# Performance work log

Measured on AMD Instinct MI355X. Metric: run time of the kernel, lower is better.

Reference implementation:

```python
import jax, jax.numpy as jnp
import numpy as np

HEADS = 4
DIM_HEAD = 32
GROUPS = 32  # min(256//4, 32)
EPS = 1e-5


def setup_inputs() -> dict:
    key = jax.random.key(0)
    ks = jax.random.split(key, 5)
    B, C, H, W = 16, 256, 64, 64
    CD, HC, WC = 512, 32, 32
    hid = HEADS * DIM_HEAD  # 128
    return {
        "x": jax.random.normal(ks[0], (B, C, H, W), jnp.float32),
        "cond": jax.random.normal(ks[1], (B, CD, HC, WC), jnp.float32),
        "gn_w": jnp.ones((C,), jnp.float32),
        "gn_b": jnp.zeros((C,), jnp.float32),
        "w_q": jax.random.normal(ks[2], (hid, C), jnp.float32) * 0.05,
        "b_q": jnp.zeros((hid,), jnp.float32),
        "w_kv": jax.random.normal(ks[3], (2 * hid, CD), jnp.float32) * 0.05,
        "b_kv": jnp.zeros((2 * hid,), jnp.float32),
        "w_out": jax.random.normal(ks[4], (C, hid), jnp.float32) * 0.05,
        "b_out": jnp.zeros((C,), jnp.float32),
    }


def _group_norm(x, w, b):
    # x: (B, C, H, W); normalize per group over (channels-in-group, H, W)
    B, C, H, W = x.shape
    xg = x.reshape(B, GROUPS, C // GROUPS, H, W)
    mu = jnp.mean(xg, axis=(2, 3, 4), keepdims=True)
    var = jnp.var(xg, axis=(2, 3, 4), keepdims=True)
    xn = ((xg - mu) * jax.lax.rsqrt(var + EPS)).reshape(B, C, H, W)
    return xn * w[None, :, None, None] + b[None, :, None, None]


def _conv1x1(x, w, b):
    # x: (B, Cin, H, W), w: (Cout, Cin), b: (Cout,)
    return jnp.einsum('oc,bchw->bohw', w, x) + b[None, :, None, None]


def reference(x, cond, gn_w, gn_b, w_q, b_q, w_kv, b_kv, w_out, b_out):
    B, C, H, W = x.shape
    hid = HEADS * DIM_HEAD
    xn = _group_norm(x, gn_w, gn_b)
    q = _conv1x1(xn, w_q, b_q)          # (B, hid, H, W)
    kv = _conv1x1(cond, w_kv, b_kv)     # (B, 2*hid, Hc, Wc)
    Nc = kv.shape[2] * kv.shape[3]
    N = H * W
    k = kv[:, :hid].reshape(B, HEADS, DIM_HEAD, Nc)
    v = kv[:, hid:].reshape(B, HEADS, DIM_HEAD, Nc)
    q = q.reshape(B, HEADS, DIM_HEAD, N)
    k = jax.nn.softmax(k, axis=-1)
    # kv outer product: (B, heads, d, e)
    context = jnp.einsum('bhdn,bhen->bhde', k, v)
    # query contraction over d: (B, heads, e, n)
    out = jnp.einsum('bhde,bhdn->bhen', context, q)
    out = out.reshape(B, hid, H, W)
    return _conv1x1(out, w_out, b_out)
```

## Files before the change

kernel.cpp:

```cpp
#include <hip/hip_runtime.h>
#include <hip/hip_bf16.h>

typedef __attribute__((ext_vector_type(8))) short bf16x8;
typedef __attribute__((ext_vector_type(4))) float f32x4;

__device__ __forceinline__ ushort f2bf(float f) {
    __hip_bfloat16 h = __float2bfloat16(f);
    return __builtin_bit_cast(ushort, h);
}
__device__ __forceinline__ float bflo(unsigned u) { return __uint_as_float(u << 16); }
__device__ __forceinline__ float bfhi(unsigned u) { return __uint_as_float(u & 0xffff0000u); }

__device__ __forceinline__ void unpack8(uint4 r, float* o) {
    o[0] = bflo(r.x); o[1] = bfhi(r.x); o[2] = bflo(r.y); o[3] = bfhi(r.y);
    o[4] = bflo(r.z); o[5] = bfhi(r.z); o[6] = bflo(r.w); o[7] = bfhi(r.w);
}

__device__ __forceinline__ void gload16(const void* g, void* l) {
    __builtin_amdgcn_global_load_lds(
        (const __attribute__((address_space(1))) unsigned*)g,
        (__attribute__((address_space(3))) unsigned*)l,
        16, 0, 0);
}

__global__ void cvtw_kernel(const float* __restrict__ w, ushort* __restrict__ o,
                            float* __restrict__ zbase) {
    int i = blockIdx.x * 256 + threadIdx.x;
    if (i < 68608) zbase[i] = 0.f;
    o[i] = f2bf(w[i]);
}

template<int C, int NPIX, bool STATS>
__device__ __forceinline__ void tconv_body(const float* __restrict__ in,
                                           ushort* __restrict__ outp,
                                           float* __restrict__ statacc,
                                           int b, int c0, int n0) {
    __shared__ ushort tile[64][68];
    __shared__ float gacc[8][2];
    const float* ip = in + (size_t)b * C * NPIX;
    ushort* op = outp + (size_t)b * NPIX * C;
    int t = threadIdx.x;
    if (STATS) {
        if (t < 16) gacc[t >> 1][t & 1] = 0.f;
        __syncthreads();
    }
    float sj[4], ssj[4];
    #pragma unroll
    for (int j = 0; j < 4; ++j) {
        int e = t + 256 * j;
        int cc = e >> 4, q = e & 15;
        float4 v = *(const float4*)&ip[(size_t)(c0 + cc) * NPIX + n0 + q * 4];
        ushort4 u;
        u.x = f2bf(v.x); u.y = f2bf(v.y); u.z = f2bf(v.z); u.w = f2bf(v.w);
        *(ushort4*)&tile[cc][q * 4] = u;
        if (STATS) {
            sj[j]  = v.x + v.y + v.z + v.w;
            ssj[j] = v.x*v.x + v.y*v.y + v.z*v.z + v.w*v.w;
        }
    }
    if (STATS) {
        #pragma unroll
        for (int j = 0; j < 4; ++j) {
            #pragma unroll
            for (int off = 1; off < 16; off <<= 1) {
                sj[j]  += __shfl_xor(sj[j], off, 64);
                ssj[j] += __shfl_xor(ssj[j], off, 64);
            }
        }
        if ((t & 15) == 0) {
            #pragma unroll
            for (int j = 0; j < 4; ++j) {
                int cc = (t >> 4) + 16 * j;
                atomicAdd(&gacc[cc >> 3][0], sj[j]);
                atomicAdd(&gacc[cc >> 3][1], ssj[j]);
            }
        }
    }
    __syncthreads();
    #pragma unroll
    for (int j = 0; j < 4; ++j) {
        int e = t + 256 * j;
        int nn = e >> 4, q = e & 15;
        ushort4 u;
        u.x = tile[q*4+0][nn]; u.y = tile[q*4+1][nn];
        u.z = tile[q*4+2][nn]; u.w = tile[q*4+3][nn];
        *(ushort4*)&op[(size_t)(n0 + nn) * C + c0 + q * 4] = u;
    }
    if (STATS && t < 8) {
        int g = b * 32 + (c0 >> 3) + t;
        atomicAdd(&statacc[g * 2],     gacc[t][0]);
        atomicAdd(&statacc[g * 2 + 1], gacc[t][1]);
    }
}

__global__ __launch_bounds__(256) void tpose_kernel(const float* __restrict__ x,
                                                    const float* __restrict__ cond,
                                                    ushort* __restrict__ xT,
                                                    ushort* __restrict__ condT,
                                                    float* __restrict__ statacc) {
    int bid = blockIdx.x;
    if (bid < 4096) {
        int b = bid >> 8, rem = bid & 255;
        tconv_body<256, 4096, true>(x, xT, statacc, b, (rem >> 6) * 64, (rem & 63) * 64);
    } else {
        int id = bid - 4096;
        int b = id >> 7, rem = id & 127;
        tconv_body<512, 1024, false>(cond, condT, nullptr, b, (rem >> 4) * 64, (rem & 15) * 64);
    }
}

template<int K, int N, bool OUTF32>
__global__ __launch_bounds__(256) void nt_gemm(const ushort* __restrict__ Amat, long long strideA,
                                               const ushort* __restrict__ Bmat, long long strideB,
                                               const float* __restrict__ biasv, int strideBias,
                                               void* __restrict__ Cmat, long long strideC) {
    __shared__ ushort lA[128 * 64];
    __shared__ ushort lB[128 * 64];
    int b = blockIdx.z;
    int col0 = blockIdx.x * 128, row0 = blockIdx.y * 128;
    int t = threadIdx.x;
    int l = t & 63, wid = t >> 6;
    int wr = wid >> 1, wc = wid & 1;
    int lr = l & 15, lg = l >> 4;
    const ushort* Ab = Amat + (size_t)b * strideA + (size_t)row0 * K;
    const ushort* Bb = Bmat + (size_t)b * strideB + (size_t)col0 * K;
    f32x4 acc[4][4] = {};
    for (int k0 = 0; k0 < K; k0 += 64) {
        #pragma unroll
        for (int j = 0; j < 4; ++j) {
            int gi = j * 256 + t;
            int r = gi >> 3, g = (gi & 7) ^ (r & 7);
            gload16(Ab + (size_t)r * K + k0 + g * 8, (char*)lA + gi * 16);
        }
        #pragma unroll
        for (int j = 0; j < 4; ++j) {
            int gi = j * 256 + t;
            int r = gi >> 3, g = (gi & 7) ^ (r & 7);
            gload16(Bb + (size_t)r * K + k0 + g * 8, (char*)lB + gi * 16);
        }
        __syncthreads();
        #pragma unroll
        for (int ks = 0; ks < 2; ++ks) {
            bf16x8 av[4], bv[4];
            #pragma unroll
            for (int mi = 0; mi < 4; ++mi) {
                int ar = wr * 64 + mi * 16 + lr;
                int q = (ks * 4 + lg) ^ (ar & 7);
                av[mi] = *(const bf16x8*)((const char*)lA + ar * 128 + q * 16);
            }
            #pragma unroll
            for (int ni = 0; ni < 4; ++ni) {
                int br = wc * 64 + ni * 16 + lr;
                int q = (ks * 4 + lg) ^ (br & 7);
                bv[ni] = *(const bf16x8*)((const char*)lB + br * 128 + q * 16);
            }
            #pragma unroll
            for (int mi = 0; mi < 4; ++mi)
                #pragma unroll
                for (int ni = 0; ni < 4; ++ni)
                    acc[mi][ni] = __builtin_amdgcn_mfma_f32_16x16x32_bf16(
                        av[mi], bv[ni], acc[mi][ni], 0, 0, 0);
        }
        __syncthreads();
    }
    const float* bp = biasv + (size_t)b * strideBias;
    int orow = row0 + wr * 64, ocol = col0 + wc * 64 + lr;
    #pragma unroll
    for (int mi = 0; mi < 4; ++mi) {
        int rb = orow + mi * 16 + lg * 4;
        float4 b4 = *(const float4*)&bp[rb];
        float bvr[4] = {b4.x, b4.y, b4.z, b4.w};
        #pragma unroll
        for (int ni = 0; ni < 4; ++ni) {
            int cc = ocol + ni * 16;
            #pragma unroll
            for (int r = 0; r < 4; ++r) {
                float v = acc[mi][ni][r] + bvr[r];
                if constexpr (OUTF32)
                    ((float*)Cmat + (size_t)b * strideC)[(size_t)(rb + r) * N + cc] = v;
                else
                    ((ushort*)Cmat + (size_t)b * strideC)[(size_t)(rb + r) * N + cc] = f2bf(v);
            }
        }
    }
}

template<int K, int N, bool OUTF32>
__global__ __launch_bounds__(256) void nt_gemm64(const ushort* __restrict__ Amat, long long strideA,
                                                 const ushort* __restrict__ Bmat, long long strideB,
                                                 const float* __restrict__ biasv, int strideBias,
                                                 void* __restrict__ Cmat, long long strideC) {
    __shared__ ushort lA[64 * 64];
    __shared__ ushort lB[64 * 64];
    int b = blockIdx.z;
    int col0 = blockIdx.x * 64, row0 = blockIdx.y * 64;
    int t = threadIdx.x;
    int l = t & 63, wid = t >> 6;
    int wr = wid >> 1, wc = wid & 1;
    int lr = l & 15, lg = l >> 4;
    const ushort* Ab = Amat + (size_t)b * strideA + (size_t)row0 * K;
    const ushort* Bb = Bmat + (size_t)b * strideB + (size_t)col0 * K;
    f32x4 acc[2][2] = {};
    for (int k0 = 0; k0 < K; k0 += 64) {
        #pragma unroll
        for (int j = 0; j < 2; ++j) {
            int gi = j * 256 + t;
            int r = gi >> 3, g = (gi & 7) ^ (r & 7);
            gload16(Ab + (size_t)r * K + k0 + g * 8, (char*)lA + gi * 16);
        }
        #pragma unroll
        for (int j = 0; j < 2; ++j) {
            int gi = j * 256 + t;
            int r = gi >> 3, g = (gi & 7) ^ (r & 7);
            gload16(Bb + (size_t)r * K + k0 + g * 8, (char*)lB + gi * 16);
        }
        __syncthreads();
        #pragma unroll
        for (int ks = 0; ks < 2; ++ks) {
            bf16x8 av[2], bv[2];
            #pragma unroll
            for (int mi = 0; mi < 2; ++mi) {
                int ar = wr * 32 + mi * 16 + lr;
                int q = (ks * 4 + lg) ^ (ar & 7);
                av[mi] = *(const bf16x8*)((const char*)lA + ar * 128 + q * 16);
            }
            #pragma unroll
            for (int ni = 0; ni < 2; ++ni) {
                int br = wc * 32 + ni * 16 + lr;
                int q = (ks * 4 + lg) ^ (br & 7);
                bv[ni] = *(const bf16x8*)((const char*)lB + br * 128 + q * 16);
            }
            #pragma unroll
            for (int mi = 0; mi < 2; ++mi)
                #pragma unroll
                for (int ni = 0; ni < 2; ++ni)
                    acc[mi][ni] = __builtin_amdgcn_mfma_f32_16x16x32_bf16(
                        av[mi], bv[ni], acc[mi][ni], 0, 0, 0);
        }
        __syncthreads();
    }
    const float* bp = biasv + (size_t)b * strideBias;
    int orow = row0 + wr * 32, ocol = col0 + wc * 32 + lr;
    #pragma unroll
    for (int mi = 0; mi < 2; ++mi) {
        int rb = orow + mi * 16 + lg * 4;
        float4 b4 = *(const float4*)&bp[rb];
        float bvr[4] = {b4.x, b4.y, b4.z, b4.w};
        #pragma unroll
        for (int ni = 0; ni < 2; ++ni) {
            int cc = ocol + ni * 16;
            #pragma unroll
            for (int r = 0; r < 4; ++r) {
                float v = acc[mi][ni][r] + bvr[r];
                if constexpr (OUTF32)
                    ((float*)Cmat + (size_t)b * strideC)[(size_t)(rb + r) * N + cc] = v;
                else
                    ((ushort*)Cmat + (size_t)b * strideC)[(size_t)(rb + r) * N + cc] = f2bf(v);
            }
        }
    }
}

__global__ __launch_bounds__(256) void ctx_partial_kernel(const ushort* __restrict__ kv,
                                                          float* __restrict__ rowsum,
                                                          float* __restrict__ ctx) {
    int bh = blockIdx.y, b = bh >> 2, h = bh & 3;
    int n0 = blockIdx.x * 128;
    __shared__ float pl[32][129], vl[32][129];
    int t = threadIdx.x;
    int r = t >> 3, cs = (t & 7) * 16;
    const ushort* kp = kv + ((size_t)b * 256 + h * 32 + r) * 1024 + n0 + cs;
    const ushort* vp = kv + ((size_t)b * 256 + 128 + h * 32 + r) * 1024 + n0 + cs;
    float kvals[16], vvals[16];
    unpack8(((const uint4*)kp)[0], kvals);
    unpack8(((const uint4*)kp)[1], kvals + 8);
    unpack8(((const uint4*)vp)[0], vvals);
    unpack8(((const uint4*)vp)[1], vvals + 8);
    float psum = 0.f;
    #pragma unroll
    for (int i = 0; i < 16; ++i) {
        float e = __expf(kvals[i]);
        pl[r][cs + i] = e;
        vl[r][cs + i] = vvals[i];
        psum += e;
    }
    psum += __shfl_xor(psum, 1, 64);
    psum += __shfl_xor(psum, 2, 64);
    psum += __shfl_xor(psum, 4, 64);
    if ((t & 7) == 0) atomicAdd(&rowsum[bh * 32 + r], psum);
    __syncthreads();
    int d0 = t >> 5, e0 = t & 31;
    float acc[4] = {0.f, 0.f, 0.f, 0.f};
    #pragma unroll 8
    for (int nn = 0; nn < 128; ++nn) {
        float vv = vl[e0][nn];
        #pragma unroll
        for (int i = 0; i < 4; ++i)
            acc[i] += pl[d0 + 8 * i][nn] * vv;
    }
    #pragma unroll
    for (int i = 0; i < 4; ++i)
        atomicAdd(&ctx[((size_t)bh * 32 + d0 + 8 * i) * 32 + e0], acc[i]);
}

__global__ __launch_bounds__(256) void a_kernel(const float* __restrict__ ctx,
                                                const float* __restrict__ rowsum,
                                                const float* __restrict__ w_out,
                                                const float* __restrict__ w_q,
                                                const float* __restrict__ b_q,
                                                const float* __restrict__ statacc,
                                                const float* __restrict__ gn_w,
                                                const float* __restrict__ gn_b,
                                                const float* __restrict__ b_out,
                                                ushort* __restrict__ A16,
                                                float* __restrict__ biasb) {
    __shared__ float ctxl[4][32][33];
    __shared__ float wol[16][128];
    __shared__ float ml[16][128];
    __shared__ float cbuf[256][17];
    __shared__ float pbuf[16][17];
    int b = blockIdx.x >> 4, ot = (blockIdx.x & 15) << 4;
    int t = threadIdx.x;
    #pragma unroll
    for (int j = 0; j < 16; ++j) {
        int e = t + 256 * j;
        float inv = 1.f / rowsum[b * 128 + (e >> 5)];
        ctxl[e >> 10][(e >> 5) & 31][e & 31] = ctx[(size_t)b * 4096 + e] * inv;
    }
    #pragma unroll
    for (int j = 0; j < 8; ++j) {
        int e = t + 256 * j;
        wol[e >> 7][e & 127] = w_out[(ot + (e >> 7)) * 128 + (e & 127)];
    }
    __syncthreads();
    #pragma unroll
    for (int j = 0; j < 8; ++j) {
        int e = t + 256 * j;
        int o = e >> 7, hd = e & 127, h = hd >> 5, d = hd & 31;
        float acc = 0.f;
        #pragma unroll
        for (int ee = 0; ee < 32; ++ee) acc += wol[o][h * 32 + ee] * ctxl[h][d][ee];
        ml[o][hd] = acc;
    }
    __syncthreads();
    int c = t, g = c >> 3;
    float a0 = statacc[(b * 32 + g) * 2], a1 = statacc[(b * 32 + g) * 2 + 1];
    float mu  = a0 * (1.f / 32768.f);
    float var = a1 * (1.f / 32768.f) - mu * mu;
    float sc = rsqrtf(var + 1e-5f) * gn_w[c];
    float tc = gn_b[c] - mu * sc;
    float wt[16];
    #pragma unroll
    for (int o = 0; o < 16; ++o) wt[o] = 0.f;
    for (int hd = 0; hd < 128; ++hd) {
        float wq = w_q[hd * 256 + c];
        #pragma unroll
        for (int o = 0; o < 16; ++o) wt[o] += ml[o][hd] * wq;
    }
    ushort* Abp = A16 + ((size_t)b * 256 + ot) * 256 + c;
    #pragma unroll
    for (int o = 0; o < 16; ++o) {
        Abp[(size_t)o * 256] = f2bf(wt[o] * sc);
        cbuf[c][o] = wt[o] * tc;
    }
    __syncthreads();
    {
        int o = t >> 4, seg = t & 15;
        float p = 0.f;
        #pragma unroll
        for (int i = 0; i < 16; ++i) p += cbuf[seg * 16 + i][o];
        pbuf[o][seg] = p;
    }
    __syncthreads();
    if (t < 16) {
        int o = t;
        float sum = 0.f;
        #pragma unroll
        for (int s2 = 0; s2 < 16; ++s2) sum += pbuf[o][s2];
        float md = 0.f;
        #pragma unroll 8
        for (int hd = 0; hd < 128; ++hd) md += ml[o][hd] * b_q[hd];
        biasb[(size_t)b * 256 + ot + o] = sum + md + b_out[ot + o];
    }
}

extern "C" void kernel_launch(void* const* d_in, const int* in_sizes, int n_in,
                              void* d_out, int out_size, void* d_ws, size_t ws_size,
                              hipStream_t stream) {
    const float* x     = (const float*)d_in[0];
    const float* cond  = (const float*)d_in[1];
    const float* gn_w  = (const float*)d_in[2];
    const float* gn_b  = (const float*)d_in[3];
    const float* w_q   = (const float*)d_in[4];
    const float* b_q   = (const float*)d_in[5];
    const float* w_kv  = (const float*)d_in[6];
    const float* b_kv  = (const float*)d_in[7];
    const float* w_out = (const float*)d_in[8];
    const float* b_out = (const float*)d_in[9];
    float* out = (float*)d_out;

    float* f       = (float*)d_ws;
    float* statacc = f;
    float* rowsum  = f + 1024;
    float* ctx     = f + 3072;
    float* biasb   = f + 68608;
    ushort* u      = (ushort*)(f + 72704);
    ushort* wkv16  = u;
    ushort* kv16   = u + 131072;
    ushort* A16    = u + 4325376;
    ushort* xT     = u + 5373952;
    ushort* condT  = u + 22151168;

    cvtw_kernel<<<512, 256, 0, stream>>>(w_kv, wkv16, statacc);
    tpose_kernel<<<6144, 256, 0, stream>>>(x, cond, xT, condT, statacc);
    nt_gemm64<512, 1024, false><<<dim3(16, 4, 16), 256, 0, stream>>>(
        wkv16, 0, condT, (long long)512 * 1024, b_kv, 0, kv16, (long long)256 * 1024);
    ctx_partial_kernel<<<dim3(8, 64), 256, 0, stream>>>(kv16, rowsum, ctx);
    a_kernel<<<256, 256, 0, stream>>>(ctx, rowsum, w_out, w_q, b_q, statacc,
                                      gn_w, gn_b, b_out, A16, biasb);
    nt_gemm<256, 4096, true><<<dim3(32, 2, 16), 256, 0, stream>>>(
        A16, 65536, xT, (long long)4096 * 256, biasb, 256, out, (long long)256 * 4096);
}
```

Before: 90.60 us.

## Fuse fp32-to-bf16 transpose into GEMM loaders and drop transpose kernel

Removes the separate transpose/convert kernel that wrote bf16 transposed copies of x and cond. Both GEMMs now read fp32 activations directly, convert them to bf16 and transpose into swizzled LDS inside the K loop. The kv GEMM kernel also computes group-norm statistics in extra blocks that read x once per group. This removes a large round-trip write and read of transposed intermediates. In exchange the loads are synchronous register loads rather than async LDS loads, and the output GEMM now uses a 256x128 tile with 512 threads.

Result: no change. 91.13 us (+0.6%).

```diff
diff --git a/kernel.cpp b/kernel.cpp
--- a/kernel.cpp
+++ b/kernel.cpp
@@ -30,233 +30,106 @@
     o[i] = f2bf(w[i]);
 }
 
-template<int C, int NPIX, bool STATS>
-__device__ __forceinline__ void tconv_body(const float* __restrict__ in,
-                                           ushort* __restrict__ outp,
-                                           float* __restrict__ statacc,
-                                           int b, int c0, int n0) {
-    __shared__ ushort tile[64][68];
-    __shared__ float gacc[8][2];
-    const float* ip = in + (size_t)b * C * NPIX;
-    ushort* op = outp + (size_t)b * NPIX * C;
-    int t = threadIdx.x;
-    if (STATS) {
-        if (t < 16) gacc[t >> 1][t & 1] = 0.f;
-        __syncthreads();
-    }
-    float sj[4], ssj[4];
-    #pragma unroll
-    for (int j = 0; j < 4; ++j) {
-        int e = t + 256 * j;
-        int cc = e >> 4, q = e & 15;
-        float4 v = *(const float4*)&ip[(size_t)(c0 + cc) * NPIX + n0 + q * 4];
-        ushort4 u;
-        u.x = f2bf(v.x); u.y = f2bf(v.y); u.z = f2bf(v.z); u.w = f2bf(v.w);
-        *(ushort4*)&tile[cc][q * 4] = u;
-        if (STATS) {
-            sj[j]  = v.x + v.y + v.z + v.w;
-            ssj[j] = v.x*v.x + v.y*v.y + v.z*v.z + v.w*v.w;
-        }
-    }
-    if (STATS) {
-        #pragma unroll
-        for (int j = 0; j < 4; ++j) {
-            #pragma unroll
-            for (int off = 1; off < 16; off <<= 1) {
-                sj[j]  += __shfl_xor(sj[j], off, 64);
-                ssj[j] += __shfl_xor(ssj[j], off, 64);
-            }
-        }
-        if ((t & 15) == 0) {
-            #pragma unroll
-            for (int j = 0; j < 4; ++j) {
-                int cc = (t >> 4) + 16 * j;
-                atomicAdd(&gacc[cc >> 3][0], sj[j]);
-                atomicAdd(&gacc[cc >> 3][1], ssj[j]);
-            }
-        }
-    }
-    __syncthreads();
-    #pragma unroll
-    for (int j = 0; j < 4; ++j) {
-        int e = t + 256 * j;
-        int nn = e >> 4, q = e & 15;
-        ushort4 u;
-        u.x = tile[q*4+0][nn]; u.y = tile[q*4+1][nn];
-        u.z = tile[q*4+2][nn]; u.w = tile[q*4+3][nn];
-        *(ushort4*)&op[(size_t)(n0 + nn) * C + c0 + q * 4] = u;
-    }
-    if (STATS && t < 8) {
-        int g = b * 32 + (c0 >> 3) + t;
-        atomicAdd(&statacc[g * 2],     gacc[t][0]);
-        atomicAdd(&statacc[g * 2 + 1], gacc[t][1]);
-    }
-}
-
-__global__ __launch_bounds__(256) void tpose_kernel(const float* __restrict__ x,
-                                                    const float* __restrict__ cond,
-                                                    ushort* __restrict__ xT,
-                                                    ushort* __restrict__ condT,
-                                                    float* __restrict__ statacc) {
-    int bid = blockIdx.x;
-    if (bid < 4096) {
-        int b = bid >> 8, rem = bid & 255;
-        tconv_body<256, 4096, true>(x, xT, statacc, b, (rem >> 6) * 64, (rem & 63) * 64);
-    } else {
-        int id = bid - 4096;
-        int b = id >> 7, rem = id & 127;
-        tconv_body<512, 1024, false>(cond, condT, nullptr, b, (rem >> 4) * 64, (rem & 15) * 64);
-    }
-}
-
-template<int K, int N, bool OUTF32>
-__global__ __launch_bounds__(256) void nt_gemm(const ushort* __restrict__ Amat, long long strideA,
-                                               const ushort* __restrict__ Bmat, long long strideB,
-                                               const float* __restrict__ biasv, int strideBias,
-                                               void* __restrict__ Cmat, long long strideC) {
-    __shared__ ushort lA[128 * 64];
-    __shared__ ushort lB[128 * 64];
-    int b = blockIdx.z;
-    int col0 = blockIdx.x * 128, row0 = blockIdx.y * 128;
-    int t = threadIdx.x;
-    int l = t & 63, wid = t >> 6;
-    int wr = wid >> 1, wc = wid & 1;
-    int lr = l & 15, lg = l >> 4;
-    const ushort* Ab = Amat + (size_t)b * strideA + (size_t)row0 * K;
-    const ushort* Bb = Bmat + (size_t)b * strideB + (size_t)col0 * K;
-    f32x4 acc[4][4] = {};
-    for (int k0 = 0; k0 < K; k0 += 64) {
-        #pragma unroll
-        for (int j = 0; j < 4; ++j) {
-            int gi = j * 256 + t;
-            int r = gi >> 3, g = (gi & 7) ^ (r & 7);
-            gload16(Ab + (size_t)r * K + k0 + g * 8, (char*)lA + gi * 16);
-        }
-        #pragma unroll
-        for (int j = 0; j < 4; ++j) {
-            int gi = j * 256 + t;
-            int r = gi >> 3, g = (gi & 7) ^ (r & 7);
-            gload16(Bb + (size_t)r * K + k0 + g * 8, (char*)lB + gi * 16);
-        }
-        __syncthreads();
-        #pragma unroll
-        for (int ks = 0; ks < 2; ++ks) {
-            bf16x8 av[4], bv[4];
-            #pragma unroll
-            for (int mi = 0; mi < 4; ++mi) {
-                int ar = wr * 64 + mi * 16 + lr;
-                int q = (ks * 4 + lg) ^ (ar & 7);
-                av[mi] = *(const bf16x8*)((const char*)lA + ar * 128 + q * 16);
-            }
-            #pragma unroll
-            for (int ni = 0; ni < 4; ++ni) {
-                int br = wc * 64 + ni * 16 + lr;
-                int q = (ks * 4 + lg) ^ (br & 7);
-                bv[ni] = *(const bf16x8*)((const char*)lB + br * 128 + q * 16);
-            }
-            #pragma unroll
-            for (int mi = 0; mi < 4; ++mi)
-                #pragma unroll
-                for (int ni = 0; ni < 4; ++ni)
-                    acc[mi][ni] = __builtin_amdgcn_mfma_f32_16x16x32_bf16(
-                        av[mi], bv[ni], acc[mi][ni], 0, 0, 0);
-        }
-        __syncthreads();
-    }
-    const float* bp = biasv + (size_t)b * strideBias;
-    int orow = row0 + wr * 64, ocol = col0 + wc * 64 + lr;
-    #pragma unroll
-    for (int mi = 0; mi < 4; ++mi) {
-        int rb = orow + mi * 16 + lg * 4;
-        float4 b4 = *(const float4*)&bp[rb];
-        float bvr[4] = {b4.x, b4.y, b4.z, b4.w};
-        #pragma unroll
-        for (int ni = 0; ni < 4; ++ni) {
-            int cc = ocol + ni * 16;
-            #pragma unroll
-            for (int r = 0; r < 4; ++r) {
-                float v = acc[mi][ni][r] + bvr[r];
-                if constexpr (OUTF32)
-                    ((float*)Cmat + (size_t)b * strideC)[(size_t)(rb + r) * N + cc] = v;
-                else
-                    ((ushort*)Cmat + (size_t)b * strideC)[(size_t)(rb + r) * N + cc] = f2bf(v);
-            }
-        }
-    }
-}
-
-template<int K, int N, bool OUTF32>
-__global__ __launch_bounds__(256) void nt_gemm64(const ushort* __restrict__ Amat, long long strideA,
-                                                 const ushort* __restrict__ Bmat, long long strideB,
-                                                 const float* __restrict__ biasv, int strideBias,
-                                                 void* __restrict__ Cmat, long long strideC) {
+__global__ __launch_bounds__(256) void kvstats_kernel(const ushort* __restrict__ wkv16,
+                                                      const float* __restrict__ cond,
+                                                      const float* __restrict__ b_kv,
+                                                      ushort* __restrict__ kv16,
+                                                      const float* __restrict__ x,
+                                                      float* __restrict__ statacc) {
     __shared__ ushort lA[64 * 64];
     __shared__ ushort lB[64 * 64];
-    int b = blockIdx.z;
-    int col0 = blockIdx.x * 64, row0 = blockIdx.y * 64;
+    __shared__ float ls[4], lss[4];
+    int bid = blockIdx.x;
     int t = threadIdx.x;
-    int l = t & 63, wid = t >> 6;
-    int wr = wid >> 1, wc = wid & 1;
-    int lr = l & 15, lg = l >> 4;
-    const ushort* Ab = Amat + (size_t)b * strideA + (size_t)row0 * K;
-    const ushort* Bb = Bmat + (size_t)b * strideB + (size_t)col0 * K;
-    f32x4 acc[2][2] = {};
-    for (int k0 = 0; k0 < K; k0 += 64) {
-        #pragma unroll
-        for (int j = 0; j < 2; ++j) {
-            int gi = j * 256 + t;
-            int r = gi >> 3, g = (gi & 7) ^ (r & 7);
-            gload16(Ab + (size_t)r * K + k0 + g * 8, (char*)lA + gi * 16);
-        }
-        #pragma unroll
-        for (int j = 0; j < 2; ++j) {
-            int gi = j * 256 + t;
-            int r = gi >> 3, g = (gi & 7) ^ (r & 7);
-            gload16(Bb + (size_t)r * K + k0 + g * 8, (char*)lB + gi * 16);
-        }
+    if (bid < 1024) {
+        int nb = bid & 15, ob = (bid >> 4) & 3, b = bid >> 6;
+        int col0 = nb * 64, row0 = ob * 64;
+        int l = t & 63, wid = t >> 6;
+        int wr = wid >> 1, wc = wid & 1;
+        int lr = l & 15, lg = l >> 4;
+        const ushort* Ab = wkv16 + (size_t)row0 * 512;
+        const float* Bb = cond + (size_t)b * 512 * 1024;
+        int sp = t & 31, sj = t >> 5;
+        f32x4 acc[2][2] = {};
+        for (int k0 = 0; k0 < 512; k0 += 64) {
+            #pragma unroll
+            for (int j = 0; j < 2; ++j) {
+                int gi = j * 256 + t;
+                int r = gi >> 3, g = (gi & 7) ^ (r & 7);
+                gload16(Ab + (size_t)r * 512 + k0 + g * 8, (char*)lA + gi * 16);
+            }
+            const float* r0 = Bb + (size_t)(k0 + 2 * sp) * 1024 + col0 + sj * 8;
+            float4 v0a = *(const float4*)r0;
+            float4 v0b = *(const float4*)(r0 + 4);
+            float4 v1a = *(const float4*)(r0 + 1024);
+            float4 v1b = *(const float4*)(r0 + 1028);
+            float c0v[8] = {v0a.x, v0a.y, v0a.z, v0a.w, v0b.x, v0b.y, v0b.z, v0b.w};
+            float c1v[8] = {v1a.x, v1a.y, v1a.z, v1a.w, v1b.x, v1b.y, v1b.z, v1b.w};
+            #pragma unroll
+            for (int w = 0; w < 8; ++w) {
+                int n = sj * 8 + w;
+                unsigned pk = (unsigned)f2bf(c0v[w]) | ((unsigned)f2bf(c1v[w]) << 16);
+                *(unsigned*)((char*)lB + n * 128 + (((sp >> 2) ^ (n & 7)) * 16) + (sp & 3) * 4) = pk;
+            }
+            __syncthreads();
+            #pragma unroll
+            for (int ks = 0; ks < 2; ++ks) {
+                bf16x8 av[2], bv[2];
+                #pragma unroll
+                for (int mi = 0; mi < 2; ++mi) {
+                    int ar = wr * 32 + mi * 16 + lr;
+                    int q = (ks * 4 + lg) ^ (ar & 7);
+                    av[mi] = *(const bf16x8*)((const char*)lA + ar * 128 + q * 16);
+                }
+                #pragma unroll
+                for (int ni = 0; ni < 2; ++ni) {
+                    int br = wc * 32 + ni * 16 + lr;
+                    int q = (ks * 4 + lg) ^ (br & 7);
+                    bv[ni] = *(const bf16x8*)((const char*)lB + br * 128 + q * 16);
+                }
+                #pragma unroll
+                for (int mi = 0; mi < 2; ++mi)
+                    #pragma unroll
+                    for (int ni = 0; ni < 2; ++ni)
+                        acc[mi][ni] = __builtin_amdgcn_mfma_f32_16x16x32_bf16(
+                            av[mi], bv[ni], acc[mi][ni], 0, 0, 0);
+            }
+            __syncthreads();
+        }
+        int orow = row0 + wr * 32, ocol = col0 + wc * 32 + lr;
+        #pragma unroll
+        for (int mi = 0; mi < 2; ++mi) {
+            int rb = orow + mi * 16 + lg * 4;
+            float4 b4 = *(const float4*)&b_kv[rb];
+            float bvr[4] = {b4.x, b4.y, b4.z, b4.w};
+            #pragma unroll
+            for (int ni = 0; ni < 2; ++ni) {
+                int cc = ocol + ni * 16;
+                #pragma unroll
+                for (int r = 0; r < 4; ++r)
+                    kv16[((size_t)b * 256 + rb + r) * 1024 + cc] = f2bf(acc[mi][ni][r] + bvr[r]);
+            }
+        }
+    } else {
+        int bg = bid - 1024;
+        const float4* xp = (const float4*)(x + (size_t)bg * 32768);
+        float s = 0.f, ss = 0.f;
+        for (int i = t; i < 8192; i += 256) {
+            float4 v = xp[i];
+            s  += v.x + v.y + v.z + v.w;
+            ss += v.x*v.x + v.y*v.y + v.z*v.z + v.w*v.w;
+        }
+        #pragma unroll
+        for (int off = 32; off > 0; off >>= 1) {
+            s  += __shfl_down(s, off, 64);
+            ss += __shfl_down(ss, off, 64);
+        }
+        int wave = t >> 6;
+        if ((t & 63) == 0) { ls[wave] = s; lss[wave] = ss; }
         __syncthreads();
-        #pragma unroll
-        for (int ks = 0; ks < 2; ++ks) {
-            bf16x8 av[2], bv[2];
-            #pragma unroll
-            for (int mi = 0; mi < 2; ++mi) {
-                int ar = wr * 32 + mi * 16 + lr;
-                int q = (ks * 4 + lg) ^ (ar & 7);
-                av[mi] = *(const bf16x8*)((const char*)lA + ar * 128 + q * 16);
-            }
-            #pragma unroll
-            for (int ni = 0; ni < 2; ++ni) {
-                int br = wc * 32 + ni * 16 + lr;
-                int q = (ks * 4 + lg) ^ (br & 7);
-                bv[ni] = *(const bf16x8*)((const char*)lB + br * 128 + q * 16);
-            }
-            #pragma unroll
-            for (int mi = 0; mi < 2; ++mi)
-                #pragma unroll
-                for (int ni = 0; ni < 2; ++ni)
-                    acc[mi][ni] = __builtin_amdgcn_mfma_f32_16x16x32_bf16(
-                        av[mi], bv[ni], acc[mi][ni], 0, 0, 0);
-        }
-        __syncthreads();
-    }
-    const float* bp = biasv + (size_t)b * strideBias;
-    int orow = row0 + wr * 32, ocol = col0 + wc * 32 + lr;
-    #pragma unroll
-    for (int mi = 0; mi < 2; ++mi) {
-        int rb = orow + mi * 16 + lg * 4;
-        float4 b4 = *(const float4*)&bp[rb];
-        float bvr[4] = {b4.x, b4.y, b4.z, b4.w};
-        #pragma unroll
-        for (int ni = 0; ni < 2; ++ni) {
-            int cc = ocol + ni * 16;
-            #pragma unroll
-            for (int r = 0; r < 4; ++r) {
-                float v = acc[mi][ni][r] + bvr[r];
-                if constexpr (OUTF32)
-                    ((float*)Cmat + (size_t)b * strideC)[(size_t)(rb + r) * N + cc] = v;
-                else
-                    ((ushort*)Cmat + (size_t)b * strideC)[(size_t)(rb + r) * N + cc] = f2bf(v);
-            }
+        if (t == 0) {
+            statacc[bg * 2]     = ls[0] + ls[1] + ls[2] + ls[3];
+            statacc[bg * 2 + 1] = lss[0] + lss[1] + lss[2] + lss[3];
         }
     }
 }
@@ -384,6 +257,84 @@
     }
 }
 
+__global__ __launch_bounds__(512) void out_gemm_fused(const ushort* __restrict__ A16,
+                                                      const float* __restrict__ x,
+                                                      const float* __restrict__ biasb,
+                                                      float* __restrict__ out) {
+    __shared__ ushort lA[256 * 64];
+    __shared__ ushort lB[128 * 64];
+    int b = blockIdx.y;
+    int n0 = blockIdx.x * 128;
+    int t = threadIdx.x;
+    int l = t & 63, wid = t >> 6;
+    int wr = wid >> 1, wc = wid & 1;
+    int lr = l & 15, lg = l >> 4;
+    const ushort* Ab = A16 + (size_t)b * 65536;
+    const float* xb = x + (size_t)b * 256 * 4096;
+    int sp = t & 31, sj = t >> 5;
+    f32x4 acc[4][4] = {};
+    for (int k0 = 0; k0 < 256; k0 += 64) {
+        #pragma unroll
+        for (int j = 0; j < 4; ++j) {
+            int gi = j * 512 + t;
+            int r = gi >> 3, g = (gi & 7) ^ (r & 7);
+            gload16(Ab + (size_t)r * 256 + k0 + g * 8, (char*)lA + gi * 16);
+        }
+        const float* r0 = xb + (size_t)(k0 + 2 * sp) * 4096 + n0 + sj * 8;
+        float4 v0a = *(const float4*)r0;
+        float4 v0b = *(const float4*)(r0 + 4);
+        float4 v1a = *(const float4*)(r0 + 4096);
+        float4 v1b = *(const float4*)(r0 + 4100);
+        float c0v[8] = {v0a.x, v0a.y, v0a.z, v0a.w, v0b.x, v0b.y, v0b.z, v0b.w};
+        float c1v[8] = {v1a.x, v1a.y, v1a.z, v1a.w, v1b.x, v1b.y, v1b.z, v1b.w};
+        #pragma unroll
+        for (int w = 0; w < 8; ++w) {
+            int n = sj * 8 + w;
+            unsigned pk = (unsigned)f2bf(c0v[w]) | ((unsigned)f2bf(c1v[w]) << 16);
+            *(unsigned*)((char*)lB + n * 128 + (((sp >> 2) ^ (n & 7)) * 16) + (sp & 3) * 4) = pk;
+        }
+        __syncthreads();
+        #pragma unroll
+        for (int ks = 0; ks < 2; ++ks) {
+            bf16x8 av[4], bv[4];
+            #pragma unroll
+            for (int mi = 0; mi < 4; ++mi) {
+                int ar = wr * 64 + mi * 16 + lr;
+                int q = (ks * 4 + lg) ^ (ar & 7);
+                av[mi] = *(const bf16x8*)((const char*)lA + ar * 128 + q * 16);
+            }
+            #pragma unroll
+            for (int ni = 0; ni < 4; ++ni) {
+                int br = wc * 64 + ni * 16 + lr;
+                int q = (ks * 4 + lg) ^ (br & 7);
+                bv[ni] = *(const bf16x8*)((const char*)lB + br * 128 + q * 16);
+            }
+            #pragma unroll
+            for (int mi = 0; mi < 4; ++mi)
+                #pragma unroll
+                for (int ni = 0; ni < 4; ++ni)
+                    acc[mi][ni] = __builtin_amdgcn_mfma_f32_16x16x32_bf16(
+                        av[mi], bv[ni], acc[mi][ni], 0, 0, 0);
+        }
+        __syncthreads();
+    }
+    const float* bp = biasb + (size_t)b * 256;
+    int orow = wr * 64, ocol = n0 + wc * 64 + lr;
+    #pragma unroll
+    for (int mi = 0; mi < 4; ++mi) {
+        int rb = orow + mi * 16 + lg * 4;
+        float4 b4 = *(const float4*)&bp[rb];
+        float bvr[4] = {b4.x, b4.y, b4.z, b4.w};
+        #pragma unroll
+        for (int ni = 0; ni < 4; ++ni) {
+            int cc = ocol + ni * 16;
+            #pragma unroll
+            for (int r = 0; r < 4; ++r)
+                out[((size_t)b * 256 + rb + r) * 4096 + cc] = acc[mi][ni][r] + bvr[r];
+        }
+    }
+}
+
 extern "C" void kernel_launch(void* const* d_in, const int* in_sizes, int n_in,
                               void* d_out, int out_size, void* d_ws, size_t ws_size,
                               hipStream_t stream) {
@@ -408,16 +359,11 @@
     ushort* wkv16  = u;
     ushort* kv16   = u + 131072;
     ushort* A16    = u + 4325376;
-    ushort* xT     = u + 5373952;
-    ushort* condT  = u + 22151168;
 
     cvtw_kernel<<<512, 256, 0, stream>>>(w_kv, wkv16, statacc);
-    tpose_kernel<<<6144, 256, 0, stream>>>(x, cond, xT, condT, statacc);
-    nt_gemm64<512, 1024, false><<<dim3(16, 4, 16), 256, 0, stream>>>(
-        wkv16, 0, condT, (long long)512 * 1024, b_kv, 0, kv16, (long long)256 * 1024);
+    kvstats_kernel<<<1536, 256, 0, stream>>>(wkv16, cond, b_kv, kv16, x, statacc);
     ctx_partial_kernel<<<dim3(8, 64), 256, 0, stream>>>(kv16, rowsum, ctx);
     a_kernel<<<256, 256, 0, stream>>>(ctx, rowsum, w_out, w_q, b_q, statacc,
                                       gn_w, gn_b, b_out, A16, biasb);
-    nt_gemm<256, 4096, true><<<dim3(32, 2, 16), 256, 0, stream>>>(
-        A16, 65536, xT, (long long)4096 * 256, biasb, 256, out, (long long)256 * 4096);
-}
+    out_gemm_fused<<<dim3(32, 16), 512, 0, stream>>>(A16, x, biasb, out);
+}
```
